# Kernel optimization log

Measured on AMD Instinct MI355X. Metric: run time of the kernel, lower is better.

The kernel has to match this reference:

```python
import jax, jax.numpy as jnp
import numpy as np

N = 100000      # nodes
E = 1600000     # directed edges (avg degree 16)
F_IN = 128
HID = 64
OUT = 10


def setup_inputs() -> dict:
    key = jax.random.key(0)
    ks = jax.random.split(key, 6)
    x = jax.random.normal(ks[0], (N, F_IN), dtype=jnp.float32)
    edge_index = jax.random.randint(ks[1], (2, E), 0, N, dtype=jnp.int32)
    # Glorot-scaled weights like PyG's GCNConv.lin; bias added post-aggregation
    W1 = jax.random.normal(ks[2], (F_IN, HID), dtype=jnp.float32) * np.float32(1.0 / np.sqrt(F_IN))
    b1 = jnp.zeros((HID,), dtype=jnp.float32)
    W2 = jax.random.normal(ks[3], (HID, OUT), dtype=jnp.float32) * np.float32(1.0 / np.sqrt(HID))
    b2 = jnp.zeros((OUT,), dtype=jnp.float32)
    return {"x": x, "edge_index": edge_index, "W1": W1, "b1": b1, "W2": W2, "b2": b2}


def _gcn_norm(edge_index, num_nodes):
    """Add self-loops and compute symmetric normalization D^-1/2 A D^-1/2 (PyG gcn_norm)."""
    loops = jnp.arange(num_nodes, dtype=edge_index.dtype)
    src = jnp.concatenate([edge_index[0], loops])
    dst = jnp.concatenate([edge_index[1], loops])
    deg = jax.ops.segment_sum(jnp.ones_like(dst, dtype=jnp.float32), dst, num_segments=num_nodes)
    dinv = jnp.where(deg > 0, jax.lax.rsqrt(deg), 0.0)  # inf -> 0 as in PyG
    norm = dinv[src] * dinv[dst]  # [E+N]
    return src, dst, norm


def _gcn_conv(x, src, dst, norm, W, b, num_nodes):
    h = x @ W                                   # transform first (smaller dim aggregated)
    msg = h[src] * norm[:, None]                # gather + scale
    agg = jax.ops.segment_sum(msg, dst, num_segments=num_nodes)  # scatter-add
    return agg + b


def reference(x, edge_index, W1, b1, W2, b2):
    src, dst, norm = _gcn_norm(edge_index, N)
    h = jax.nn.relu(_gcn_conv(x, src, dst, norm, W1, b1, N))
    # F.dropout(training=self.training): identity in eval mode
    out = _gcn_conv(h, src, dst, norm, W2, b2, N)
    return out
```

## Files before the change

kernel.cpp:

```cpp
#include <hip/hip_runtime.h>
#include <hip/hip_fp16.h>

static constexpr int F = 128;
static constexpr int H = 64;
static constexpr int O = 10;
static constexpr int PSU = 6;
static constexpr int NBUK_MAX = 256;
static constexpr int CAP = 12288;
static constexpr int ESCAP = 14336;
static constexpr int EPB = 4096;
static constexpr int XPAD = 136;

typedef _Float16 half8 __attribute__((ext_vector_type(8)));
typedef float floatx4 __attribute__((ext_vector_type(4)));

__global__ __launch_bounds__(256) void k_init(int* __restrict__ bcntg,
                                              const float* __restrict__ W1,
                                              __half* __restrict__ W1f,
                                              unsigned* __restrict__ yN,
                                              unsigned* __restrict__ zsN) {
    int b = blockIdx.x, t = threadIdx.x;
    if (b == 0) {
        bcntg[t] = 0;
        if (t < 32) yN[t] = 0u;
        if (t < PSU) zsN[t] = 0u;
    } else {
        int i = (b - 1) * 256 + t;
        int j = i & 7, lane = (i >> 3) & 63, sc = i >> 9;
        int s = sc >> 2, c = sc & 3;
        int k = s * 32 + (lane >> 4) * 8 + j;
        int nn = c * 16 + (lane & 15);
        W1f[i] = __float2half(W1[k * H + nn]);
    }
}

__global__ __launch_bounds__(256) void k_bin(const int* __restrict__ src,
                                             const int* __restrict__ dst,
                                             int* __restrict__ bcntg,
                                             unsigned* __restrict__ ebuf, int e_total) {
    __shared__ int hist[NBUK_MAX];
    __shared__ int base[NBUK_MAX];
    __shared__ int loc[NBUK_MAX];
    int t = threadIdx.x;
    hist[t] = 0;
    loc[t] = 0;
    __syncthreads();
    int i0 = blockIdx.x * EPB;
    int i1 = min(i0 + EPB, e_total);
    int i = i0 + 4 * t;
    for (; i + 3 < i1; i += 1024) {
        int4 d4 = *(const int4*)&dst[i];
        atomicAdd(&hist[d4.x >> 9], 1);
        atomicAdd(&hist[d4.y >> 9], 1);
        atomicAdd(&hist[d4.z >> 9], 1);
        atomicAdd(&hist[d4.w >> 9], 1);
    }
    for (; i < i1; ++i) atomicAdd(&hist[dst[i] >> 9], 1);
    __syncthreads();
    if (hist[t] > 0) base[t] = atomicAdd(&bcntg[t], hist[t]);
    __syncthreads();
    i = i0 + 4 * t;
    for (; i + 3 < i1; i += 1024) {
        int4 s4 = *(const int4*)&src[i];
        int4 d4 = *(const int4*)&dst[i];
#pragma unroll
        for (int u = 0; u < 4; ++u) {
            int s = (&s4.x)[u], d = (&d4.x)[u];
            int b = d >> 9;
            int r = base[b] + atomicAdd(&loc[b], 1);
            if (r < CAP)
                ebuf[(size_t)b * CAP + r] = ((unsigned)(d & 511) << 17) | (unsigned)s;
        }
    }
    for (; i < i1; ++i) {
        int s = src[i], d = dst[i];
        int b = d >> 9;
        int r = base[b] + atomicAdd(&loc[b], 1);
        if (r < CAP)
            ebuf[(size_t)b * CAP + r] = ((unsigned)(d & 511) << 17) | (unsigned)s;
    }
}

__global__ __launch_bounds__(256) void k_bsort(
    const unsigned* __restrict__ ebuf, const int* __restrict__ bcntg,
    int* __restrict__ rowbeg, int* __restrict__ degp, float* __restrict__ dinv,
    int* __restrict__ esrc, int n_nodes) {
    __shared__ int hc[512];
    __shared__ int sa[512];
    __shared__ int sb[512];
    int t = threadIdx.x, b = blockIdx.x, n0 = b << 9;
    hc[t] = 0;
    hc[t + 256] = 0;
    __syncthreads();
    int cb = min(bcntg[b], CAP);
    const unsigned* eb = ebuf + (size_t)b * CAP;
    int i = 4 * t;
    for (; i + 3 < cb; i += 1024) {
        uint4 e4 = *(const uint4*)&eb[i];
        atomicAdd(&hc[e4.x >> 17], 1);
        atomicAdd(&hc[e4.y >> 17], 1);
        atomicAdd(&hc[e4.z >> 17], 1);
        atomicAdd(&hc[e4.w >> 17], 1);
    }
    for (; i < cb; ++i) atomicAdd(&hc[eb[i] >> 17], 1);
    __syncthreads();
#pragma unroll
    for (int u = 0; u < 2; ++u) {
        int ii = t + 256 * u;
        sa[ii] = (hc[ii] + 15) & ~15;
    }
    __syncthreads();
    int* A = sa;
    int* Bp = sb;
    for (int off = 1; off < 512; off <<= 1) {
#pragma unroll
        for (int u = 0; u < 2; ++u) {
            int ii = t + 256 * u;
            int v = A[ii];
            if (ii >= off) v += A[ii - off];
            Bp[ii] = v;
        }
        __syncthreads();
        int* tmp = A; A = Bp; Bp = tmp;
    }
#pragma unroll
    for (int u = 0; u < 2; ++u) {
        int ii = t + 256 * u;
        int cnt = hc[ii];
        int cp = (cnt + 15) & ~15;
        int excl = A[ii] - cp;
        Bp[ii] = excl;
        int n = n0 + ii;
        if (n < n_nodes) {
            rowbeg[n] = b * ESCAP + excl;
            degp[n] = cp;
            dinv[n] = rsqrtf((float)cnt + 1.0f);
        }
    }
    __syncthreads();
    int* es = esrc + (size_t)b * ESCAP;
    i = 4 * t;
    for (; i + 3 < cb; i += 1024) {
        uint4 e4 = *(const uint4*)&eb[i];
#pragma unroll
        for (int u = 0; u < 4; ++u) {
            unsigned e = (&e4.x)[u];
            int r = atomicAdd(&Bp[e >> 17], 1);
            es[r] = (int)(e & 0x1FFFFu);
        }
    }
    for (; i < cb; ++i) {
        unsigned e = eb[i];
        int r = atomicAdd(&Bp[e >> 17], 1);
        es[r] = (int)(e & 0x1FFFFu);
    }
    __syncthreads();
#pragma unroll
    for (int u = 0; u < 2; ++u) {
        int ii = t + 256 * u;
        int end = A[ii];
        for (int p = Bp[ii]; p < end; ++p) es[p] = n_nodes;
    }
}

__global__ __launch_bounds__(256, 4) void k_gemm1(
    const float* __restrict__ x, const __half* __restrict__ W1f,
    const float* __restrict__ dinv, __half* __restrict__ y, int n_nodes) {
    __shared__ __half xh[64 * XPAD];
    const int tid = threadIdx.x;
    const int lane = tid & 63;
    const int w = tid >> 6;
    const int row0 = blockIdx.x * 64;

    half8 bf[16];
    const uint4* wf = (const uint4*)W1f;
#pragma unroll
    for (int sc = 0; sc < 16; ++sc) {
        union { uint4 u; half8 h; } tmp;
        tmp.u = wf[sc * 64 + lane];
        bf[sc] = tmp.h;
    }

    for (int i = tid; i < 64 * 32; i += 256) {
        int r = i >> 5, k4 = i & 31;
        int gr = row0 + r;
        if (gr < n_nodes) {
            float4 v = *(const float4*)&x[(size_t)gr * F + 4 * k4];
            __half2 p0 = __floats2half2_rn(v.x, v.y);
            __half2 p1 = __floats2half2_rn(v.z, v.w);
            uint2 pk = make_uint2(*(unsigned*)&p0, *(unsigned*)&p1);
            *(uint2*)&xh[r * XPAD + 4 * k4] = pk;
        }
    }
    __syncthreads();

    const int m16 = lane & 15, quad = lane >> 4;
    floatx4 acc[4];
#pragma unroll
    for (int c = 0; c < 4; ++c) acc[c] = (floatx4){0.f, 0.f, 0.f, 0.f};
#pragma unroll
    for (int s = 0; s < 4; ++s) {
        union { uint4 u; half8 h; } ua;
        ua.u = *(const uint4*)&xh[(16 * w + m16) * XPAD + s * 32 + quad * 8];
#pragma unroll
        for (int c = 0; c < 4; ++c)
            acc[c] = __builtin_amdgcn_mfma_f32_16x16x32_f16(ua.h, bf[s * 4 + c],
                                                            acc[c], 0, 0, 0);
    }
#pragma unroll
    for (int r = 0; r < 4; ++r) {
        int grow = row0 + 16 * w + quad * 4 + r;
        if (grow < n_nodes) {
            float d = dinv[grow];
#pragma unroll
            for (int c = 0; c < 4; ++c)
                y[(size_t)grow * H + c * 16 + m16] = __float2half(acc[c][r] * d);
        }
    }
}

__global__ __launch_bounds__(256) void k_gather1z(
    const uint4* __restrict__ yq4, const int* __restrict__ rowbeg,
    const int* __restrict__ degp, const int* __restrict__ esrc,
    const float* __restrict__ dinv, const float* __restrict__ b1,
    const float* __restrict__ W2, unsigned* __restrict__ zs_u, int n_nodes) {
    __shared__ float w2t[O * H];
    for (int i = threadIdx.x; i < O * H; i += 256)
        w2t[i] = W2[(i & 63) * O + (i >> 6)];
    __syncthreads();
    const int l = threadIdx.x & 63;
    const int c = l & 7;
    const int gbase = l & ~7;
    const int n = blockIdx.x * 32 + (threadIdx.x >> 3);
    if (n >= n_nodes) return;
    const int beg = rowbeg[n];
    const int dp = degp[n];
    const float d = dinv[n];

    float acc[8];
    {
        uint4 v = yq4[(size_t)n * 8 + c];
        float2 f0 = __half22float2(*(const __half2*)&v.x);
        float2 f1 = __half22float2(*(const __half2*)&v.y);
        float2 f2 = __half22float2(*(const __half2*)&v.z);
        float2 f3 = __half22float2(*(const __half2*)&v.w);
        acc[0] = f0.x; acc[1] = f0.y; acc[2] = f1.x; acc[3] = f1.y;
        acc[4] = f2.x; acc[5] = f2.y; acc[6] = f3.x; acc[7] = f3.y;
    }
    for (int k0 = 0; k0 < dp; k0 += 16) {
        int2 idx = *(const int2*)&esrc[beg + k0 + 2 * c];
#pragma unroll
        for (int e = 0; e < 16; ++e) {
            int s = __shfl((e & 1) ? idx.y : idx.x, gbase + (e >> 1), 64);
            uint4 v = yq4[(size_t)s * 8 + c];
            float2 f0 = __half22float2(*(const __half2*)&v.x);
            float2 f1 = __half22float2(*(const __half2*)&v.y);
            float2 f2 = __half22float2(*(const __half2*)&v.z);
            float2 f3 = __half22float2(*(const __half2*)&v.w);
            acc[0] += f0.x; acc[1] += f0.y; acc[2] += f1.x; acc[3] += f1.y;
            acc[4] += f2.x; acc[5] += f2.y; acc[6] += f3.x; acc[7] += f3.y;
        }
    }
    const float4 ba = ((const float4*)b1)[2 * c];
    const float4 bbv = ((const float4*)b1)[2 * c + 1];
    float h[8];
    h[0] = fmaxf(fmaf(d, acc[0], ba.x), 0.0f);
    h[1] = fmaxf(fmaf(d, acc[1], ba.y), 0.0f);
    h[2] = fmaxf(fmaf(d, acc[2], ba.z), 0.0f);
    h[3] = fmaxf(fmaf(d, acc[3], ba.w), 0.0f);
    h[4] = fmaxf(fmaf(d, acc[4], bbv.x), 0.0f);
    h[5] = fmaxf(fmaf(d, acc[5], bbv.y), 0.0f);
    h[6] = fmaxf(fmaf(d, acc[6], bbv.z), 0.0f);
    h[7] = fmaxf(fmaf(d, acc[7], bbv.w), 0.0f);
    float p[O];
#pragma unroll
    for (int j = 0; j < O; ++j) {
        float4 wa = *(const float4*)&w2t[j * 64 + 8 * c];
        float4 wb = *(const float4*)&w2t[j * 64 + 8 * c + 4];
        p[j] = h[0] * wa.x + h[1] * wa.y + h[2] * wa.z + h[3] * wa.w
             + h[4] * wb.x + h[5] * wb.y + h[6] * wb.z + h[7] * wb.w;
    }
#pragma unroll
    for (int m = 1; m <= 4; m <<= 1) {
#pragma unroll
        for (int j = 0; j < O; ++j) p[j] += __shfl_xor(p[j], m, 64);
    }
    if (c == 0) {
        __half2 q0 = __floats2half2_rn(p[0] * d, p[1] * d);
        __half2 q1 = __floats2half2_rn(p[2] * d, p[3] * d);
        __half2 q2 = __floats2half2_rn(p[4] * d, p[5] * d);
        __half2 q3 = __floats2half2_rn(p[6] * d, p[7] * d);
        __half2 q4 = __floats2half2_rn(p[8] * d, p[9] * d);
        uint2* zp = (uint2*)&zs_u[(size_t)n * PSU];
        zp[0] = make_uint2(*(const unsigned*)&q0, *(const unsigned*)&q1);
        zp[1] = make_uint2(*(const unsigned*)&q2, *(const unsigned*)&q3);
        zp[2] = make_uint2(*(const unsigned*)&q4, 0u);
    }
}

__global__ __launch_bounds__(256) void k_gather2(
    const unsigned* __restrict__ zs_u, const int* __restrict__ rowbeg,
    const int* __restrict__ degp, const int* __restrict__ esrc,
    const float* __restrict__ dinv, const float* __restrict__ b2,
    float* __restrict__ out, int n_nodes) {
    const int l = threadIdx.x & 63;
    const int j = l & 7;
    const int sbase = l & ~7;
    const int jj = (j < 5) ? j : 5;
    const int n = blockIdx.x * 32 + (threadIdx.x >> 3);
    if (n >= n_nodes) return;
    const int beg = rowbeg[n];
    const int dp = degp[n];
    unsigned v0 = zs_u[(size_t)n * PSU + jj];
    float2 acc = __half22float2(*(const __half2*)&v0);
    for (int k0 = 0; k0 < dp; k0 += 8) {
        int idx = esrc[beg + k0 + j];
#pragma unroll
        for (int e = 0; e < 8; ++e) {
            int s = __shfl(idx, sbase + e, 64);
            unsigned v = zs_u[(size_t)s * PSU + jj];
            float2 f = __half22float2(*(const __half2*)&v);
            acc.x += f.x;
            acc.y += f.y;
        }
    }
    if (j < 5) {
        float2 bb = ((const float2*)b2)[j];
        float d = dinv[n];
        float2 o = make_float2(fmaf(d, acc.x, bb.x), fmaf(d, acc.y, bb.y));
        *(float2*)&out[(size_t)n * O + 2 * j] = o;
    }
}

static inline size_t align256(size_t v) { return (v + 255) & ~(size_t)255; }

extern "C" void kernel_launch(void* const* d_in, const int* in_sizes, int n_in,
                              void* d_out, int out_size, void* d_ws, size_t ws_size,
                              hipStream_t stream) {
    const float* x  = (const float*)d_in[0];
    const int*   ei = (const int*)d_in[1];
    const float* W1 = (const float*)d_in[2];
    const float* b1 = (const float*)d_in[3];
    const float* W2 = (const float*)d_in[4];
    const float* b2 = (const float*)d_in[5];
    float* out = (float*)d_out;

    const int N = in_sizes[0] / F;
    const int E = in_sizes[1] / 2;
    const int* src = ei;
    const int* dst = ei + E;
    const int NBUK = (N + 511) >> 9;

    char* base = (char*)d_ws;
    __half* y = (__half*)base;
    size_t ysz = align256((size_t)(N + 1) * H * 2);
    char* hreg = base + ysz;
    unsigned* ebuf = (unsigned*)hreg;
    __half* W1f = (__half*)(hreg + (size_t)N * H * 2 - (size_t)F * H * 2);
    size_t hsz = align256((size_t)N * H * 2);
    char* zreg = hreg + hsz;
    unsigned* zs_u = (unsigned*)zreg;
    size_t zsz = align256((size_t)(N + 1) * PSU * 4);
    float* dinv = (float*)(zreg + zsz);
    int* rowbeg = (int*)(dinv + N);
    int* degp = rowbeg + N;
    int* bcntg = degp + N;
    int* esrc = bcntg + 256;

    const int nb_bin = (E + EPB - 1) / EPB;

    k_init<<<1 + F * H / 256, 256, 0, stream>>>(bcntg, W1, W1f,
                                                (unsigned*)(y + (size_t)N * H),
                                                zs_u + (size_t)N * PSU);
    k_bin<<<nb_bin, 256, 0, stream>>>(src, dst, bcntg, ebuf, E);
    k_bsort<<<NBUK, 256, 0, stream>>>(ebuf, bcntg, rowbeg, degp, dinv, esrc, N);
    k_gemm1<<<(N + 63) / 64, 256, 0, stream>>>(x, W1f, dinv, y, N);
    k_gather1z<<<(N + 31) / 32, 256, 0, stream>>>((const uint4*)y, rowbeg, degp,
                                                  esrc, dinv, b1, W2, zs_u, N);
    k_gather2<<<(N + 31) / 32, 256, 0, stream>>>(zs_u, rowbeg, degp, esrc,
                                                 dinv, b2, out, N);
}
```

Measured before the change: 189.9 us.

## Pad adjacency rows to 8 and use 4 lanes per node in layer-2 gather

```diff
diff --git a/kernel.cpp b/kernel.cpp
--- a/kernel.cpp
+++ b/kernel.cpp
@@ -107,7 +107,7 @@
 #pragma unroll
     for (int u = 0; u < 2; ++u) {
         int ii = t + 256 * u;
-        sa[ii] = (hc[ii] + 15) & ~15;
+        sa[ii] = (hc[ii] + 7) & ~7;
     }
     __syncthreads();
     int* A = sa;
@@ -127,7 +127,7 @@
     for (int u = 0; u < 2; ++u) {
         int ii = t + 256 * u;
         int cnt = hc[ii];
-        int cp = (cnt + 15) & ~15;
+        int cp = (cnt + 7) & ~7;
         int excl = A[ii] - cp;
         Bp[ii] = excl;
         int n = n0 + ii;
@@ -247,11 +247,11 @@
         acc[0] = f0.x; acc[1] = f0.y; acc[2] = f1.x; acc[3] = f1.y;
         acc[4] = f2.x; acc[5] = f2.y; acc[6] = f3.x; acc[7] = f3.y;
     }
-    for (int k0 = 0; k0 < dp; k0 += 16) {
-        int2 idx = *(const int2*)&esrc[beg + k0 + 2 * c];
-#pragma unroll
-        for (int e = 0; e < 16; ++e) {
-            int s = __shfl((e & 1) ? idx.y : idx.x, gbase + (e >> 1), 64);
+    for (int k0 = 0; k0 < dp; k0 += 8) {
+        int idx = esrc[beg + k0 + c];
+#pragma unroll
+        for (int e = 0; e < 8; ++e) {
+            int s = __shfl(idx, gbase + e, 64);
             uint4 v = yq4[(size_t)s * 8 + c];
             float2 f0 = __half22float2(*(const __half2*)&v.x);
             float2 f1 = __half22float2(*(const __half2*)&v.y);
@@ -304,31 +304,38 @@
     const float* __restrict__ dinv, const float* __restrict__ b2,
     float* __restrict__ out, int n_nodes) {
     const int l = threadIdx.x & 63;
-    const int j = l & 7;
-    const int sbase = l & ~7;
-    const int jj = (j < 5) ? j : 5;
-    const int n = blockIdx.x * 32 + (threadIdx.x >> 3);
+    const int j = l & 3;
+    const int gb = l & ~3;
+    const int jj = (j < 3) ? j : 2;
+    const int n = blockIdx.x * 64 + (threadIdx.x >> 2);
     if (n >= n_nodes) return;
     const int beg = rowbeg[n];
     const int dp = degp[n];
-    unsigned v0 = zs_u[(size_t)n * PSU + jj];
-    float2 acc = __half22float2(*(const __half2*)&v0);
+    uint2 v0 = *(const uint2*)&zs_u[(size_t)n * PSU + 2 * jj];
+    float2 accA = __half22float2(*(const __half2*)&v0.x);
+    float2 accB = __half22float2(*(const __half2*)&v0.y);
     for (int k0 = 0; k0 < dp; k0 += 8) {
-        int idx = esrc[beg + k0 + j];
+        int2 idx = *(const int2*)&esrc[beg + k0 + 2 * j];
 #pragma unroll
         for (int e = 0; e < 8; ++e) {
-            int s = __shfl(idx, sbase + e, 64);
-            unsigned v = zs_u[(size_t)s * PSU + jj];
-            float2 f = __half22float2(*(const __half2*)&v);
-            acc.x += f.x;
-            acc.y += f.y;
-        }
-    }
-    if (j < 5) {
-        float2 bb = ((const float2*)b2)[j];
-        float d = dinv[n];
-        float2 o = make_float2(fmaf(d, acc.x, bb.x), fmaf(d, acc.y, bb.y));
-        *(float2*)&out[(size_t)n * O + 2 * j] = o;
+            int s = __shfl((e & 1) ? idx.y : idx.x, gb + (e >> 1), 64);
+            uint2 v = *(const uint2*)&zs_u[(size_t)s * PSU + 2 * jj];
+            float2 fA = __half22float2(*(const __half2*)&v.x);
+            float2 fB = __half22float2(*(const __half2*)&v.y);
+            accA.x += fA.x; accA.y += fA.y;
+            accB.x += fB.x; accB.y += fB.y;
+        }
+    }
+    if (j < 3) {
+        const float d = dinv[n];
+        float2 bbA = ((const float2*)b2)[2 * j];
+        float2 oA = make_float2(fmaf(d, accA.x, bbA.x), fmaf(d, accA.y, bbA.y));
+        *(float2*)&out[(size_t)n * O + 4 * j] = oA;
+        if (j < 2) {
+            float2 bbB = ((const float2*)b2)[2 * j + 1];
+            float2 oB = make_float2(fmaf(d, accB.x, bbB.x), fmaf(d, accB.y, bbB.y));
+            *(float2*)&out[(size_t)n * O + 4 * j + 2] = oB;
+        }
     }
 }
 
@@ -377,6 +384,6 @@
     k_gemm1<<<(N + 63) / 64, 256, 0, stream>>>(x, W1f, dinv, y, N);
     k_gather1z<<<(N + 31) / 32, 256, 0, stream>>>((const uint4*)y, rowbeg, degp,
                                                   esrc, dinv, b1, W2, zs_u, N);
-    k_gather2<<<(N + 31) / 32, 256, 0, stream>>>(zs_u, rowbeg, degp, esrc,
+    k_gather2<<<(N + 63) / 64, 256, 0, stream>>>(zs_u, rowbeg, degp, esrc,
                                                  dinv, b2, out, N);
 }
```

Measured after the change: 189.7 us, median of 2. Within noise of the previous version (-0.1%).
